# Optimization experiments

Hardware: AMD Instinct MI355X
Metric: run time of the kernel (lower is better)

## Reference

```python
import jax, jax.numpy as jnp
import numpy as np

B, S, N = 8, 2048, 1024

def setup_inputs() -> dict:
    key = jax.random.key(0)
    k1, k2, k3 = jax.random.split(key, 3)
    outer = jax.random.normal(k1, (B, S, N), dtype=jnp.float32)
    extended_attention_mask = jnp.zeros((B, 1, S), dtype=jnp.float32)
    # torch Linear init scale ~ 1/sqrt(n)
    sc = 1.0 / np.sqrt(N)
    Wk = jax.random.normal(k2, (N, N), dtype=jnp.float32) * sc
    bk = jnp.zeros((N,), dtype=jnp.float32)
    Wq = jax.random.normal(k3, (N, N), dtype=jnp.float32) * sc
    bq = jnp.zeros((N,), dtype=jnp.float32)
    return {"outer": outer, "extended_attention_mask": extended_attention_mask,
            "Wk": Wk, "bk": bk, "Wq": Wq, "bq": bq}

def reference(outer, extended_attention_mask, Wk, bk, Wq, bq):
    # k = sigmoid(outer @ Wk^T + bk), q = sigmoid(outer @ Wq^T + bq)
    k = jax.nn.sigmoid(jnp.einsum('bsn,mn->bsm', outer, Wk) + bk)  # [B,S,N]
    q = jax.nn.sigmoid(jnp.einsum('bsn,mn->bsm', outer, Wq) + bq)  # [B,S,N]
    # scores: q @ k^T + mask -> [B,S,S]
    s = jnp.einsum('bqn,bkn->bqk', q, k) + extended_attention_mask
    attn = jax.nn.softmax(s, axis=-1)
    out = jnp.einsum('bqk,bkn->bqn', attn, outer)  # [B,S,N]
    return out.sum(-1)  # [B,S]
```

## Files before the change

### kernel.cpp

```cpp
#include <hip/hip_runtime.h>
#include <hip/hip_bf16.h>

#define BB 8
#define SS 2048
#define NN 1024
#define MT (BB*SS)
#define NPC 32
#define NT 16

typedef __attribute__((ext_vector_type(8))) short bf16x8;
typedef __attribute__((ext_vector_type(4))) float f32x4;
typedef unsigned short u16;
typedef unsigned int u32;

__device__ __forceinline__ u16 f2bf(float f) {
  u32 u = __float_as_uint(f);
  u += 0x7fff + ((u >> 16) & 1);
  return (u16)(u >> 16);
}
__device__ __forceinline__ float bf2f(u16 h) {
  return __uint_as_float(((u32)h) << 16);
}

typedef __attribute__((address_space(1))) void GV;
typedef __attribute__((address_space(3))) void LV;
__device__ __forceinline__ void cp16(const void* g, void* l) {
  __builtin_amdgcn_global_load_lds((GV*)g, (LV*)l, 16, 0, 0);
}

#define WAIT4 asm volatile("s_waitcnt vmcnt(4)" ::: "memory")
#define WAIT6 asm volatile("s_waitcnt vmcnt(6)" ::: "memory")
#define LGKM0 asm volatile("s_waitcnt lgkmcnt(0)" ::: "memory")
#define BARX  __builtin_amdgcn_s_barrier()
#define SCB0  __builtin_amdgcn_sched_barrier(0)

__global__ __launch_bounds__(256) void prep_x_kernel(const float* __restrict__ outer,
                                                     const float* __restrict__ mask,
                                                     u16* __restrict__ Xb,
                                                     float* __restrict__ r,
                                                     float* __restrict__ kb) {
  int w = threadIdx.x >> 6, lane = threadIdx.x & 63;
  int row = blockIdx.x * 4 + w;
  const float4* src = (const float4*)(outer + (size_t)row * NN);
  ushort4* dst = (ushort4*)(Xb + (size_t)row * NN);
  float s = 0.f;
#pragma unroll
  for (int u = 0; u < 4; u++) {
    int idx = lane + u * 64;
    float4 v = src[idx];
    ushort4 o;
    o.x = f2bf(v.x); o.y = f2bf(v.y); o.z = f2bf(v.z); o.w = f2bf(v.w);
    dst[idx] = o;
    s += (v.x + v.y) + (v.z + v.w);
  }
#pragma unroll
  for (int off = 1; off < 64; off <<= 1) s += __shfl_xor(s, off);
  if (lane == 0) { r[row] = s; kb[row] = mask[row]; }
}

__global__ __launch_bounds__(256) void prep_w_kernel(const float* __restrict__ Wq,
                                                     const float* __restrict__ Wk,
                                                     const float* __restrict__ bq,
                                                     const float* __restrict__ bk,
                                                     u16* __restrict__ Wb,
                                                     float* __restrict__ bb) {
  int idx = blockIdx.x * 256 + threadIdx.x;
  int e = idx * 4;
  int rowm = e >> 10;
  int col = e & 1023;
  const float* srcp = (rowm < NN) ? (Wq + (size_t)rowm * NN + col)
                                  : (Wk + (size_t)(rowm - NN) * NN + col);
  float4 v = *(const float4*)srcp;
  ushort4 o; o.x = f2bf(v.x); o.y = f2bf(v.y); o.z = f2bf(v.z); o.w = f2bf(v.w);
  *(ushort4*)(Wb + (size_t)e) = o;
  if (idx < 2 * NN) bb[idx] = (idx < NN) ? bq[idx] : bk[idx - NN];
}

template<int LDG>
__device__ __forceinline__ void gemm_core(const u16* gA, const u16* gB,
                                          u16* lds, int tid,
                                          f32x4 (&acc)[8][4]) {
  const int lane = tid & 63, w = tid >> 6;
  const int wr = w >> 2, wc = w & 3;
  const int l15 = lane & 15, quad = lane >> 4, xq = l15 & 7;
  const int lr = lane >> 3, lc = lane & 7;
  const int sslot = lc ^ lr;
  const int so0 = ((quad ^ xq)) * 8;
  const int so1 = (((4 + quad) ^ xq)) * 8;

  const u16* gAr = gA + (size_t)(wr * 128 + wc * 8 + lr) * LDG + sslot * 8;
  const u16* gBr = gB + (size_t)(wc * 64 + wr * 8 + lr) * LDG + sslot * 8;

  auto STA = [&](int buf, int lo, int kt) {
    cp16(gAr + (size_t)lo * 32 * LDG + kt * 64,
         lds + buf * 32768 + wr * 8192 + ((lo * 4 + wc) * 64 + lane) * 8);
  };
  auto STB = [&](int buf, int lb, int kt) {
    cp16(gBr + (size_t)lb * 16 * LDG + kt * 64,
         lds + buf * 32768 + 16384 + wc * 4096 + ((lb * 2 + wr) * 64 + lane) * 8);
  };

  bf16x8 af[4][2], bf[2][2];
  auto LDA4 = [&](int buf, int ih) {
#pragma unroll
    for (int i2 = 0; i2 < 4; ++i2) {
      const u16* p = lds + buf * 32768 + wr * 8192 + (ih * 64 + i2 * 16 + l15) * 64;
      af[i2][0] = *(const bf16x8*)(p + so0);
      af[i2][1] = *(const bf16x8*)(p + so1);
    }
  };
  auto LDB2 = [&](int buf, int jh) {
#pragma unroll
    for (int j2 = 0; j2 < 2; ++j2) {
      const u16* p = lds + buf * 32768 + 16384 + wc * 4096 + ((jh * 2 + j2) * 16 + l15) * 64;
      bf[j2][0] = *(const bf16x8*)(p + so0);
      bf[j2][1] = *(const bf16x8*)(p + so1);
    }
  };
  auto MQ = [&](int ih, int jh) {
    __builtin_amdgcn_s_setprio(1);
#pragma unroll
    for (int ks = 0; ks < 2; ++ks)
#pragma unroll
      for (int i2 = 0; i2 < 4; ++i2)
#pragma unroll
        for (int j2 = 0; j2 < 2; ++j2)
          acc[ih * 4 + i2][jh * 2 + j2] =
              __builtin_amdgcn_mfma_f32_16x16x32_bf16(af[i2][ks], bf[j2][ks],
                                                      acc[ih * 4 + i2][jh * 2 + j2], 0, 0, 0);
    __builtin_amdgcn_s_setprio(0);
  };

  STA(0, 0, 0); STA(0, 1, 0); STB(0, 0, 0); STB(0, 1, 0);
  STB(0, 2, 0); STB(0, 3, 0); STA(0, 2, 0); STA(0, 3, 0);
  WAIT4; BARX;

#pragma unroll 1
  for (int t = 0; t < NT; ++t) {
    const int buf = t & 1, nb = buf ^ 1, nt = t + 1;
    const bool st = (t < NT - 1);
    LDA4(buf, 0); LDB2(buf, 0);
    if (st) { STA(nb, 0, nt); STA(nb, 1, nt); }
    WAIT4; BARX; LGKM0; SCB0;
    MQ(0, 0);
    BARX;
    LDB2(buf, 1);
    if (st) { STB(nb, 0, nt); STB(nb, 1, nt); }
    WAIT4; BARX; LGKM0; SCB0;
    MQ(0, 1);
    BARX;
    LDA4(buf, 1);
    if (st) { STB(nb, 2, nt); STB(nb, 3, nt); }
    WAIT6; BARX; LGKM0; SCB0;
    MQ(1, 1);
    BARX;
    LDB2(buf, 0);
    if (st) { STA(nb, 2, nt); STA(nb, 3, nt); }
    WAIT4; BARX; LGKM0; SCB0;
    MQ(1, 0);
    BARX;
  }
}

__global__ __launch_bounds__(512, 2) void gemm1_kernel(const u16* __restrict__ X,
                                                       const u16* __restrict__ W,
                                                       const float* __restrict__ bb,
                                                       u16* __restrict__ C,
                                                       float* __restrict__ kb) {
  __shared__ u16 lds[2 * 32768];
  int bid = blockIdx.x;
  int xcd = bid & 7, idx = bid >> 3;
  int tm = xcd * 8 + (idx & 7);
  int tn = idx >> 3;
  int tid = threadIdx.x;
  f32x4 acc[8][4] = {};
  gemm_core<1024>(X + (size_t)tm * 256 * 1024, W + (size_t)tn * 256 * 1024,
                  lds, tid, acc);

  int lane = tid & 63, w = tid >> 6;
  int wr = w >> 2, wc = w & 3, l15 = lane & 15, quad = lane >> 4;
  int colb = tn * 256 + wc * 64 + l15;
  bool khalf = (tn >= 4);
  int rowb = tm * 256 + wr * 128 + quad * 4;
#pragma unroll
  for (int i = 0; i < 8; ++i) {
    float rsum[4] = {0.f, 0.f, 0.f, 0.f};
#pragma unroll
    for (int j = 0; j < 4; ++j) {
      int col = colb + j * 16;
      float bias = bb[col];
#pragma unroll
      for (int rg = 0; rg < 4; ++rg) {
        int row = rowb + i * 16 + rg;
        float v = acc[i][j][rg] + bias;
        float sg = 1.0f / (1.0f + __expf(-v));
        u16 h = f2bf(sg - 0.5f);
        C[(size_t)row * 2048 + col] = h;
        rsum[rg] += bf2f(h);
      }
    }
    if (khalf) {
#pragma unroll
      for (int rg = 0; rg < 4; ++rg) {
        float s = rsum[rg];
#pragma unroll
        for (int off = 1; off < 16; off <<= 1) s += __shfl_xor(s, off);
        if (l15 == 0) atomicAdd(&kb[rowb + i * 16 + rg], 0.5f * s);
      }
    }
  }
}

__global__ __launch_bounds__(512, 2) void flash_kernel(const u16* __restrict__ Cq,
                                                       const float* __restrict__ kb,
                                                       const float* __restrict__ r,
                                                       float* __restrict__ pm,
                                                       float* __restrict__ pl,
                                                       float* __restrict__ pt) {
  __shared__ u16 lds[2 * 32768];
  int bid = blockIdx.x;
  int b = bid & 7;
  int idx = bid >> 3;
  int qt = idx >> 3;
  int kc = idx & 7;
  int tid = threadIdx.x;
  f32x4 acc[8][4] = {};
  gemm_core<2048>(Cq + (size_t)(b * SS + qt * 256) * 2048,
                  Cq + (size_t)(b * SS + kc * 256) * 2048 + 1024,
                  lds, tid, acc);

  int lane = tid & 63, w = tid >> 6;
  int wr = w >> 2, wc = w & 3, l15 = lane & 15, quad = lane >> 4;
  float kbv[4], rv[4];
  int colg = b * SS + kc * 256 + wc * 64 + l15;
#pragma unroll
  for (int j = 0; j < 4; ++j) { kbv[j] = kb[colg + j * 16]; rv[j] = r[colg + j * 16]; }
  int chunk = kc * 4 + wc;
  int rowb = b * SS + qt * 256 + wr * 128 + quad * 4;
#pragma unroll
  for (int i = 0; i < 8; ++i) {
#pragma unroll
    for (int rg = 0; rg < 4; ++rg) {
      float lg[4];
      float tmax = -1e30f;
#pragma unroll
      for (int j = 0; j < 4; ++j) { lg[j] = acc[i][j][rg] + kbv[j]; tmax = fmaxf(tmax, lg[j]); }
#pragma unroll
      for (int off = 1; off < 16; off <<= 1) tmax = fmaxf(tmax, __shfl_xor(tmax, off));
      float rs = 0.f, rt = 0.f;
#pragma unroll
      for (int j = 0; j < 4; ++j) {
        float p = __expf(lg[j] - tmax);
        rs += p; rt += p * rv[j];
      }
#pragma unroll
      for (int off = 1; off < 16; off <<= 1) { rs += __shfl_xor(rs, off); rt += __shfl_xor(rt, off); }
      if (l15 == 0) {
        int grow = rowb + i * 16 + rg;
        pm[(size_t)grow * NPC + chunk] = tmax;
        pl[(size_t)grow * NPC + chunk] = rs;
        pt[(size_t)grow * NPC + chunk] = rt;
      }
    }
  }
}

__global__ __launch_bounds__(256) void fixup_kernel(const float* __restrict__ pm,
                                                    const float* __restrict__ pl,
                                                    const float* __restrict__ pt,
                                                    float* __restrict__ out) {
  int row = blockIdx.x * 256 + threadIdx.x;
  float Mx = -1e30f;
#pragma unroll
  for (int c = 0; c < NPC; c++) Mx = fmaxf(Mx, pm[row * NPC + c]);
  float L = 0.f, T = 0.f;
#pragma unroll
  for (int c = 0; c < NPC; c++) {
    float a = __expf(pm[row * NPC + c] - Mx);
    L += pl[row * NPC + c] * a;
    T += pt[row * NPC + c] * a;
  }
  out[row] = T / L;
}

extern "C" void kernel_launch(void* const* d_in, const int* in_sizes, int n_in,
                              void* d_out, int out_size, void* d_ws, size_t ws_size,
                              hipStream_t stream) {
  const float* outer = (const float*)d_in[0];
  const float* mask  = (const float*)d_in[1];
  const float* Wk    = (const float*)d_in[2];
  const float* bk    = (const float*)d_in[3];
  const float* Wq    = (const float*)d_in[4];
  const float* bq    = (const float*)d_in[5];
  float* out = (float*)d_out;

  char* ws = (char*)d_ws;
  size_t off = 0;
  auto alloc = [&](size_t bytes) -> void* {
    void* p = ws + off;
    off = (off + bytes + 255) & ~(size_t)255;
    return p;
  };
  u16* Xb  = (u16*)alloc((size_t)MT * NN * 2);
  u16* Wb  = (u16*)alloc((size_t)2048 * NN * 2);
  u16* Cq  = (u16*)alloc((size_t)MT * 2048 * 2);
  float* bb = (float*)alloc(2048 * 4);
  float* rr = (float*)alloc((size_t)MT * 4);
  float* kb = (float*)alloc((size_t)MT * 4);
  float* pm = (float*)alloc((size_t)MT * NPC * 4);
  float* pl = (float*)alloc((size_t)MT * NPC * 4);
  float* pt = (float*)alloc((size_t)MT * NPC * 4);

  prep_x_kernel<<<dim3(MT / 4), dim3(256), 0, stream>>>(outer, mask, Xb, rr, kb);
  prep_w_kernel<<<dim3(2048), dim3(256), 0, stream>>>(Wq, Wk, bq, bk, Wb, bb);
  gemm1_kernel<<<dim3(512), dim3(512), 0, stream>>>(Xb, Wb, bb, Cq, kb);
  flash_kernel<<<dim3(512), dim3(512), 0, stream>>>(Cq, kb, rr, pm, pl, pt);
  fixup_kernel<<<dim3(MT / 256), dim3(256), 0, stream>>>(pm, pl, pt, out);
}
```

Before: 283.9 us.

## Restructure GEMM LDS pipeline with early prefetch into freed buffer regions

Rewrites the double-buffered GEMM main loop so global-to-LDS copies for tile t+2 are issued into the current buffer as soon as its A/B halves have been consumed, and tile t+1 copies go out earlier. It keeps two B fragment register sets so the B LDS reload before the last MFMA quadrant is dropped, and most per-phase vmcnt waits are removed. Addresses are precomputed and advanced incrementally, and the loop is unrolled by two buffers. This aims to deepen the prefetch distance and cut waits and LDS reads, at the cost of more VGPRs and a more delicate ordering of waits and barriers.

```diff
diff --git a/kernel.cpp b/kernel.cpp
--- a/kernel.cpp
+++ b/kernel.cpp
@@ -29,7 +29,7 @@
 }
 
 #define WAIT4 asm volatile("s_waitcnt vmcnt(4)" ::: "memory")
-#define WAIT6 asm volatile("s_waitcnt vmcnt(6)" ::: "memory")
+#define WAIT0 asm volatile("s_waitcnt vmcnt(0)" ::: "memory")
 #define LGKM0 asm volatile("s_waitcnt lgkmcnt(0)" ::: "memory")
 #define BARX  __builtin_amdgcn_s_barrier()
 #define SCB0  __builtin_amdgcn_sched_barrier(0)
@@ -85,39 +85,36 @@
   const int l15 = lane & 15, quad = lane >> 4, xq = l15 & 7;
   const int lr = lane >> 3, lc = lane & 7;
   const int sslot = lc ^ lr;
-  const int so0 = ((quad ^ xq)) * 8;
-  const int so1 = (((4 + quad) ^ xq)) * 8;
+  const int so0 = (quad ^ xq) * 8;
+  const int so1 = ((4 + quad) ^ xq) * 8;
 
   const u16* gAr = gA + (size_t)(wr * 128 + wc * 8 + lr) * LDG + sslot * 8;
   const u16* gBr = gB + (size_t)(wc * 64 + wr * 8 + lr) * LDG + sslot * 8;
 
-  auto STA = [&](int buf, int lo, int kt) {
-    cp16(gAr + (size_t)lo * 32 * LDG + kt * 64,
-         lds + buf * 32768 + wr * 8192 + ((lo * 4 + wc) * 64 + lane) * 8);
-  };
-  auto STB = [&](int buf, int lb, int kt) {
-    cp16(gBr + (size_t)lb * 16 * LDG + kt * 64,
-         lds + buf * 32768 + 16384 + wc * 4096 + ((lb * 2 + wr) * 64 + lane) * 8);
-  };
-
-  bf16x8 af[4][2], bf[2][2];
-  auto LDA4 = [&](int buf, int ih) {
+  u16* dA = lds + wr * 8192 + (wc * 64 + lane) * 8;
+  u16* dB = lds + 16384 + wc * 4096 + wr * 512 + lane * 8;
+  const u16* pA = lds + wr * 8192 + l15 * 64;
+  const u16* pB = lds + 16384 + wc * 4096 + l15 * 64;
+
+  bf16x8 af[4][2], bf0[2][2], bf1[2][2];
+
+  auto LDA = [&](int buf, int ih) {
 #pragma unroll
     for (int i2 = 0; i2 < 4; ++i2) {
-      const u16* p = lds + buf * 32768 + wr * 8192 + (ih * 64 + i2 * 16 + l15) * 64;
+      const u16* p = pA + buf * 32768 + (ih * 64 + i2 * 16) * 64;
       af[i2][0] = *(const bf16x8*)(p + so0);
       af[i2][1] = *(const bf16x8*)(p + so1);
     }
   };
-  auto LDB2 = [&](int buf, int jh) {
+  auto LDB = [&](int buf, int jh, bf16x8 (&bf)[2][2]) {
 #pragma unroll
     for (int j2 = 0; j2 < 2; ++j2) {
-      const u16* p = lds + buf * 32768 + 16384 + wc * 4096 + ((jh * 2 + j2) * 16 + l15) * 64;
+      const u16* p = pB + buf * 32768 + (jh * 2 + j2) * 1024;
       bf[j2][0] = *(const bf16x8*)(p + so0);
       bf[j2][1] = *(const bf16x8*)(p + so1);
     }
   };
-  auto MQ = [&](int ih, int jh) {
+  auto MQ = [&](int ih, int jh, bf16x8 (&bf)[2][2]) {
     __builtin_amdgcn_s_setprio(1);
 #pragma unroll
     for (int ks = 0; ks < 2; ++ks)
@@ -131,34 +128,60 @@
     __builtin_amdgcn_s_setprio(0);
   };
 
-  STA(0, 0, 0); STA(0, 1, 0); STB(0, 0, 0); STB(0, 1, 0);
-  STB(0, 2, 0); STB(0, 3, 0); STA(0, 2, 0); STA(0, 3, 0);
+#pragma unroll
+  for (int lo = 0; lo < 4; ++lo) cp16(gAr + (size_t)lo * 32 * LDG, dA + lo * 2048);
+#pragma unroll
+  for (int lb = 0; lb < 4; ++lb) cp16(gBr + (size_t)lb * 16 * LDG, dB + lb * 1024);
+  cp16(gAr + 64,                          dA + 32768);
+  cp16(gAr + (size_t)32 * LDG + 64,       dA + 32768 + 2048);
+  cp16(gBr + (size_t)2 * 16 * LDG + 64,   dB + 32768 + 2048);
+  cp16(gBr + (size_t)3 * 16 * LDG + 64,   dB + 32768 + 3072);
   WAIT4; BARX;
 
+  const u16 *a1 = gAr + 64, *b1 = gBr + 64, *a2 = gAr + 128, *b2 = gBr + 128;
+
+  auto TILE = [&](int buf, bool st1, bool st2) {
+    const int nb = buf ^ 1;
+    LDA(buf, 0); LDB(buf, 0, bf0);
+    if (st1) {
+      cp16(a1 + (size_t)2 * 32 * LDG, dA + nb * 32768 + 2 * 2048);
+      cp16(a1 + (size_t)3 * 32 * LDG, dA + nb * 32768 + 3 * 2048);
+      cp16(b1,                        dB + nb * 32768);
+      cp16(b1 + (size_t)16 * LDG,     dB + nb * 32768 + 1024);
+    }
+    BARX; LGKM0; SCB0;
+    MQ(0, 0, bf0);
+    BARX;
+    LDB(buf, 1, bf1);
+    BARX; LGKM0; SCB0;
+    MQ(0, 1, bf1);
+    BARX;
+    LDA(buf, 1);
+    if (st2) {
+      cp16(a2,                        dA + buf * 32768);
+      cp16(a2 + (size_t)32 * LDG,     dA + buf * 32768 + 2048);
+    }
+    BARX; LGKM0; SCB0;
+    MQ(1, 1, bf1);
+    BARX;
+    if (st2) {
+      cp16(b2 + (size_t)2 * 16 * LDG, dB + buf * 32768 + 2048);
+      cp16(b2 + (size_t)3 * 16 * LDG, dB + buf * 32768 + 3072);
+      WAIT4;
+    } else {
+      WAIT0;
+    }
+    BARX;
+    MQ(1, 0, bf0);
+    BARX;
+    a1 += 64; b1 += 64; a2 += 64; b2 += 64;
+  };
+
 #pragma unroll 1
-  for (int t = 0; t < NT; ++t) {
-    const int buf = t & 1, nb = buf ^ 1, nt = t + 1;
-    const bool st = (t < NT - 1);
-    LDA4(buf, 0); LDB2(buf, 0);
-    if (st) { STA(nb, 0, nt); STA(nb, 1, nt); }
-    WAIT4; BARX; LGKM0; SCB0;
-    MQ(0, 0);
-    BARX;
-    LDB2(buf, 1);
-    if (st) { STB(nb, 0, nt); STB(nb, 1, nt); }
-    WAIT4; BARX; LGKM0; SCB0;
-    MQ(0, 1);
-    BARX;
-    LDA4(buf, 1);
-    if (st) { STB(nb, 2, nt); STB(nb, 3, nt); }
-    WAIT6; BARX; LGKM0; SCB0;
-    MQ(1, 1);
-    BARX;
-    LDB2(buf, 0);
-    if (st) { STA(nb, 2, nt); STA(nb, 3, nt); }
-    WAIT4; BARX; LGKM0; SCB0;
-    MQ(1, 0);
-    BARX;
+  for (int tt = 0; tt < 8; ++tt) {
+    bool nl = (tt != 7);
+    TILE(0, true, nl);
+    TILE(1, nl, nl);
   }
 }
 
```

After: 270.9 us. 4.6% less time.
